# Optimization experiments

Measured on AMD Instinct MI355X. Metric: run time of the kernel, lower is better.

## Reference

```python
import jax, jax.numpy as jnp
import numpy as np

N_NODES = 50000
EMBED = 64
N_EDGES = 1250000
N_USERS = 25000
BATCH, K = 1024, 100


def setup_inputs() -> dict:
    key = jax.random.key(0)
    ks = jax.random.split(key, 8)
    stdv = 1.0 / np.sqrt(EMBED)
    emb = jax.random.uniform(ks[0], (N_NODES, EMBED), jnp.float32, -stdv, stdv)
    # nn.Linear default init: U(-1/sqrt(fan_in), 1/sqrt(fan_in))
    lim = 1.0 / np.sqrt(EMBED)
    W0 = jax.random.uniform(ks[1], (EMBED, EMBED), jnp.float32, -lim, lim)
    b0 = jax.random.uniform(ks[2], (EMBED,), jnp.float32, -lim, lim)
    W1 = jax.random.uniform(ks[3], (EMBED, EMBED), jnp.float32, -lim, lim)
    b1 = jax.random.uniform(ks[4], (EMBED,), jnp.float32, -lim, lim)
    src = jax.random.randint(ks[5], (N_EDGES,), 0, N_NODES, jnp.int32)
    dst = jax.random.randint(ks[6], (N_EDGES,), 0, N_NODES, jnp.int32)
    user_index = jax.random.randint(ks[7], (BATCH, K), 0, N_USERS, jnp.int32)
    item_index = jax.random.randint(jax.random.fold_in(key, 99), (BATCH, K), 0, N_NODES, jnp.int32)
    return {"embeddings": emb, "W0": W0, "b0": b0, "W1": W1, "b1": b1,
            "src": src, "dst": dst, "user_index": user_index, "item_index": item_index}


def _mean_aggregate(h, src, dst):
    # copy_src gather + mailbox mean: mean of src features over incoming edges per dst
    msg_sum = jax.ops.segment_sum(h[src], dst, num_segments=N_NODES)  # [N, D]
    deg = jax.ops.segment_sum(jnp.ones((src.shape[0],), h.dtype), dst, num_segments=N_NODES)
    return msg_sum / jnp.maximum(deg, 1.0)[:, None]


def reference(embeddings, W0, b0, W1, b1, src, dst, user_index, item_index):
    h = embeddings
    for W, b in ((W0, b0), (W1, b1)):
        agg = _mean_aggregate(h, src, dst)          # [N, D] mean mailbox
        h = jnp.tanh(agg @ W.T + b)                  # NodeUpdate: Linear + Tanh
    user = h[user_index]                             # [B, K, D]
    item = h[item_index]                             # [B, K, D]
    score = jnp.sum(user * item, axis=2)             # [B, K]
    return score
```

## Files before the change

kernel.cpp:

```cpp
#include <hip/hip_runtime.h>

#define N_NODES 50000
#define N_EDGES 1250000
#define EMBED 64
#define N_PAIRS (1024 * 100)
#define BSHIFT 7
#define BSIZE 128
#define NBUCK 391
#define CB 153
#define LDS_CAP 4096
#define GEMV_BLKS ((N_NODES + 63) / 64)

__device__ inline float bf2f(unsigned short u) {
    return __uint_as_float(((unsigned)u) << 16);
}
__device__ inline unsigned short f2bf(float x) {
    unsigned u = __float_as_uint(x);
    u += 0x7FFF + ((u >> 16) & 1);
    return (unsigned short)(u >> 16);
}

__global__ __launch_bounds__(1024) void hist_kernel(const int* __restrict__ dst,
                                                    int* __restrict__ counts) {
    __shared__ int hl[NBUCK];
    int t = threadIdx.x, b = blockIdx.x;
    for (int i = t; i < NBUCK; i += 1024) hl[i] = 0;
    __syncthreads();
    #pragma unroll
    for (int rep = 0; rep < 2; ++rep) {
        int i4 = b * 2048 + rep * 1024 + t;
        if (i4 < N_EDGES / 4) {
            int4 d = ((const int4*)dst)[i4];
            atomicAdd(&hl[d.x >> BSHIFT], 1);
            atomicAdd(&hl[d.y >> BSHIFT], 1);
            atomicAdd(&hl[d.z >> BSHIFT], 1);
            atomicAdd(&hl[d.w >> BSHIFT], 1);
        }
    }
    __syncthreads();
    for (int i = t; i < NBUCK; i += 1024) counts[i * CB + b] = hl[i];
}

__global__ __launch_bounds__(512) void prep_kernel(const int* __restrict__ counts,
                                                   int* __restrict__ offs,
                                                   int* __restrict__ base) {
    __shared__ int ws[8];
    int t = threadIdx.x, lane = t & 63, wid = t >> 6;
    const int* rowp = counts + (size_t)t * CB;
    int tot = 0;
    if (t < NBUCK)
        for (int b = 0; b < CB; ++b) tot += rowp[b];
    int incl = tot;
    #pragma unroll
    for (int off = 1; off < 64; off <<= 1) {
        int o = __shfl_up(incl, off);
        if (lane >= off) incl += o;
    }
    if (lane == 63) ws[wid] = incl;
    __syncthreads();
    if (t < 8) {
        int x = ws[t];
        #pragma unroll
        for (int off = 1; off < 8; off <<= 1) {
            int o = __shfl_up(x, off);
            if (t >= off) x += o;
        }
        ws[t] = x;
    }
    __syncthreads();
    int ex = ((wid > 0) ? ws[wid - 1] : 0) + incl - tot;
    if (t < NBUCK) base[t] = ex;
    if (t == 0) base[NBUCK] = N_EDGES;
    if (t < NBUCK) {
        int run = ex;
        int* orow = offs + (size_t)t * CB;
        for (int b = 0; b < CB; ++b) {
            orow[b] = run;
            run += rowp[b];
        }
    }
}

__global__ __launch_bounds__(1024) void scatter_kernel(const int* __restrict__ src,
                                                       const int* __restrict__ dst,
                                                       const int* __restrict__ offs,
                                                       unsigned int* __restrict__ pairs) {
    __shared__ int cur[NBUCK];
    int t = threadIdx.x, b = blockIdx.x;
    for (int i = t; i < NBUCK; i += 1024) cur[i] = offs[i * CB + b];
    __syncthreads();
    #pragma unroll
    for (int rep = 0; rep < 2; ++rep) {
        int i4 = b * 2048 + rep * 1024 + t;
        if (i4 < N_EDGES / 4) {
            int4 s4 = ((const int4*)src)[i4];
            int4 d4 = ((const int4*)dst)[i4];
            int p;
            p = atomicAdd(&cur[d4.x >> BSHIFT], 1);
            pairs[p] = ((unsigned)(d4.x & (BSIZE - 1)) << 16) | (unsigned)s4.x;
            p = atomicAdd(&cur[d4.y >> BSHIFT], 1);
            pairs[p] = ((unsigned)(d4.y & (BSIZE - 1)) << 16) | (unsigned)s4.y;
            p = atomicAdd(&cur[d4.z >> BSHIFT], 1);
            pairs[p] = ((unsigned)(d4.z & (BSIZE - 1)) << 16) | (unsigned)s4.z;
            p = atomicAdd(&cur[d4.w >> BSHIFT], 1);
            pairs[p] = ((unsigned)(d4.w & (BSIZE - 1)) << 16) | (unsigned)s4.w;
        }
    }
}

#define SMEM_BYTES 33808
__global__ __launch_bounds__(256) void sortgemv_kernel(const unsigned int* __restrict__ pairs,
                                                       const int* __restrict__ base,
                                                       int* __restrict__ row,
                                                       int* __restrict__ col,
                                                       const float* __restrict__ emb,
                                                       const float* __restrict__ W,
                                                       unsigned short* __restrict__ g) {
    __shared__ __align__(16) char smem[SMEM_BYTES];
    int t = threadIdx.x;
    if (blockIdx.x < NBUCK) {
        unsigned* ebuf = (unsigned*)smem;
        int* staged    = (int*)(smem + 16384);
        int* hist      = (int*)(smem + 32768);
        int* cur       = (int*)(smem + 33280);
        int* wtot      = (int*)(smem + 33792);
        int k = blockIdx.x;
        int lane = t & 63, wid = t >> 6;
        int nstart = k * BSIZE;
        int nodes = min(BSIZE, N_NODES - nstart);
        int estart = base[k], eend = base[k + 1];
        int cnt = eend - estart;
        if (t < BSIZE) hist[t] = 0;
        __syncthreads();
        if (cnt <= LDS_CAP) {
            for (int i = t; i < cnt; i += 256) {
                unsigned w = pairs[estart + i];
                ebuf[i] = w;
                atomicAdd(&hist[w >> 16], 1);
            }
            __syncthreads();
            if (t < BSIZE) {
                int v = hist[t];
                int incl = v;
                #pragma unroll
                for (int off = 1; off < 64; off <<= 1) {
                    int o = __shfl_up(incl, off);
                    if (lane >= off) incl += o;
                }
                if (t == 63) *wtot = incl;
                __syncthreads();
                int ex = incl - v + ((wid == 1) ? *wtot : 0);
                cur[t] = ex;
                if (t < nodes) row[nstart + t] = estart + ex;
            } else {
                __syncthreads();
            }
            if (k == NBUCK - 1 && t == 0) row[N_NODES] = N_EDGES;
            __syncthreads();
            for (int i = t; i < cnt; i += 256) {
                unsigned w = ebuf[i];
                int pos = atomicAdd(&cur[w >> 16], 1);
                staged[pos] = (int)(w & 0xFFFFu);
            }
            __syncthreads();
            for (int i = t; i < cnt; i += 256) col[estart + i] = staged[i];
        } else {
            for (int i = t; i < cnt; i += 256)
                atomicAdd(&hist[pairs[estart + i] >> 16], 1);
            __syncthreads();
            if (t < BSIZE) {
                int v = hist[t];
                int incl = v;
                #pragma unroll
                for (int off = 1; off < 64; off <<= 1) {
                    int o = __shfl_up(incl, off);
                    if (lane >= off) incl += o;
                }
                if (t == 63) *wtot = incl;
                __syncthreads();
                int ex = incl - v + ((wid == 1) ? *wtot : 0);
                cur[t] = ex;
                if (t < nodes) row[nstart + t] = estart + ex;
            } else {
                __syncthreads();
            }
            if (k == NBUCK - 1 && t == 0) row[N_NODES] = N_EDGES;
            __syncthreads();
            for (int i = t; i < cnt; i += 256) {
                unsigned w = pairs[estart + i];
                int pos = atomicAdd(&cur[w >> 16], 1);
                col[estart + pos] = (int)(w & 0xFFFFu);
            }
        }
    } else {
        float (*hL)[64] = (float (*)[64])smem;
        float (*Wl)[65] = (float (*)[65])(smem + 16384);
        int nstart = (blockIdx.x - NBUCK) * 64;
        int lane = t & 63, wid = t >> 6;
        for (int i = t; i < 4096; i += 256) Wl[i & 63][i >> 6] = W[i];
        int nrem = min(64, N_NODES - nstart);
        for (int i = t; i < nrem * 16; i += 256)
            ((float4*)hL)[i] = ((const float4*)(emb + (size_t)nstart * EMBED))[i];
        __syncthreads();
        for (int n = wid; n < nrem; n += 4) {
            float x = 0.f;
            #pragma unroll
            for (int d = 0; d < 64; ++d)
                x += hL[n][d] * Wl[d][lane];
            g[(size_t)(nstart + n) * EMBED + lane] = f2bf(x);
        }
    }
}

__global__ __launch_bounds__(256) void gemv_bf16_kernel(const unsigned short* __restrict__ h,
                                                        const float* __restrict__ W,
                                                        unsigned short* __restrict__ g) {
    __shared__ float hL[64][64];
    __shared__ float Wl[64][65];
    int t = threadIdx.x;
    int nstart = blockIdx.x * 64;
    int lane = t & 63, wid = t >> 6;
    for (int i = t; i < 4096; i += 256) Wl[i & 63][i >> 6] = W[i];
    int nrem = min(64, N_NODES - nstart);
    for (int i = t; i < nrem * 16; i += 256) {
        ushort4 v = ((const ushort4*)(h + (size_t)nstart * EMBED))[i];
        int r = i >> 4, c = (i & 15) * 4;
        hL[r][c + 0] = bf2f(v.x);
        hL[r][c + 1] = bf2f(v.y);
        hL[r][c + 2] = bf2f(v.z);
        hL[r][c + 3] = bf2f(v.w);
    }
    __syncthreads();
    for (int n = wid; n < nrem; n += 4) {
        float x = 0.f;
        #pragma unroll
        for (int d = 0; d < 64; ++d)
            x += hL[n][d] * Wl[d][lane];
        g[(size_t)(nstart + n) * EMBED + lane] = f2bf(x);
    }
}

__global__ __launch_bounds__(256) void agg_kernel(const unsigned short* __restrict__ g,
                                                  const float* __restrict__ bias,
                                                  const int* __restrict__ row,
                                                  const int* __restrict__ col,
                                                  unsigned short* __restrict__ hout) {
    int t = threadIdx.x;
    int wid = t >> 6, lane = t & 63;
    int node = blockIdx.x * 4 + wid;
    int gg = lane >> 4, d16 = lane & 15;
    int start = row[node], end = row[node + 1];
    float4 bb = ((const float4*)bias)[d16];
    float4 acc = {0.f, 0.f, 0.f, 0.f};
    for (int e = start; e < end; e += 32) {
        #pragma unroll
        for (int k = 0; k < 8; ++k) {
            int ee = e + 4 * k + gg;
            if (ee < end) {
                int s = col[ee];
                ushort4 v = ((const ushort4*)(g + (size_t)s * EMBED))[d16];
                acc.x += bf2f(v.x);
                acc.y += bf2f(v.y);
                acc.z += bf2f(v.z);
                acc.w += bf2f(v.w);
            }
        }
    }
    #pragma unroll
    for (int off = 16; off < 64; off <<= 1) {
        acc.x += __shfl_xor(acc.x, off);
        acc.y += __shfl_xor(acc.y, off);
        acc.z += __shfl_xor(acc.z, off);
        acc.w += __shfl_xor(acc.w, off);
    }
    int dg = end - start;
    float inv = (dg > 0) ? 1.0f / (float)dg : 0.f;
    if (gg == 0) {
        ushort4 o;
        o.x = f2bf(tanhf(acc.x * inv + bb.x));
        o.y = f2bf(tanhf(acc.y * inv + bb.y));
        o.z = f2bf(tanhf(acc.z * inv + bb.z));
        o.w = f2bf(tanhf(acc.w * inv + bb.w));
        ((ushort4*)(hout + (size_t)node * EMBED))[d16] = o;
    }
}

__global__ __launch_bounds__(256) void score_kernel(const unsigned short* __restrict__ h,
                                                    const int* __restrict__ ui,
                                                    const int* __restrict__ ii,
                                                    float* __restrict__ out) {
    int t = threadIdx.x;
    int idx = blockIdx.x * 16 + (t >> 4);
    int d16 = t & 15;
    int u = ui[idx];
    int v = ii[idx];
    ushort4 a4 = ((const ushort4*)(h + (size_t)u * EMBED))[d16];
    ushort4 b4 = ((const ushort4*)(h + (size_t)v * EMBED))[d16];
    float p = bf2f(a4.x) * bf2f(b4.x) + bf2f(a4.y) * bf2f(b4.y) +
              bf2f(a4.z) * bf2f(b4.z) + bf2f(a4.w) * bf2f(b4.w);
    #pragma unroll
    for (int off = 8; off > 0; off >>= 1)
        p += __shfl_xor(p, off);
    if (d16 == 0) out[idx] = p;
}

extern "C" void kernel_launch(void* const* d_in, const int* in_sizes, int n_in,
                              void* d_out, int out_size, void* d_ws, size_t ws_size,
                              hipStream_t stream) {
    const float* emb = (const float*)d_in[0];
    const float* W0  = (const float*)d_in[1];
    const float* b0  = (const float*)d_in[2];
    const float* W1  = (const float*)d_in[3];
    const float* b1  = (const float*)d_in[4];
    const int* src   = (const int*)d_in[5];
    const int* dst   = (const int*)d_in[6];
    const int* ui    = (const int*)d_in[7];
    const int* ii    = (const int*)d_in[8];
    float* out = (float*)d_out;

    char* p = (char*)d_ws;
    auto alloc = [&](size_t bytes) {
        char* r = p;
        p += (bytes + 255) & ~(size_t)255;
        return r;
    };
    int* counts          = (int*)alloc(sizeof(int) * NBUCK * CB);
    int* offs            = (int*)alloc(sizeof(int) * NBUCK * CB);
    int* base            = (int*)alloc(sizeof(int) * (NBUCK + 1));
    int* row             = (int*)alloc(sizeof(int) * (N_NODES + 1));
    unsigned* pairs      = (unsigned*)alloc(sizeof(unsigned) * N_EDGES);
    int* col             = (int*)alloc(sizeof(int) * N_EDGES);
    unsigned short* gbuf = (unsigned short*)alloc(sizeof(unsigned short) * N_NODES * EMBED);
    unsigned short* hbuf = (unsigned short*)alloc(sizeof(unsigned short) * N_NODES * EMBED);

    hist_kernel<<<CB, 1024, 0, stream>>>(dst, counts);
    prep_kernel<<<1, 512, 0, stream>>>(counts, offs, base);
    scatter_kernel<<<CB, 1024, 0, stream>>>(src, dst, offs, pairs);
    sortgemv_kernel<<<NBUCK + GEMV_BLKS, 256, 0, stream>>>(pairs, base, row, col,
                                                           emb, W0, gbuf);
    agg_kernel<<<N_NODES / 4, 256, 0, stream>>>(gbuf, b0, row, col, hbuf);
    gemv_bf16_kernel<<<GEMV_BLKS, 256, 0, stream>>>(hbuf, W1, gbuf);
    agg_kernel<<<N_NODES / 4, 256, 0, stream>>>(gbuf, b1, row, col, hbuf);
    score_kernel<<<N_PAIRS / 16, 256, 0, stream>>>(hbuf, ui, ii, out);
}
```

Measured before the change: 257.7 us.

## Parallelize bucket offset scan across blocks with atomic totals and warp scans

The single-block prep kernel is split up. Bucket totals are now accumulated with global atomics in the histogram kernel, a small single-block kernel scans those totals, and a new kernel with one 64-thread block per bucket computes the per-block offsets using wavefront shuffle scans. This removes the serial per-thread loops over 153 entries in one block, which read the counts with strided, uncoalesced access. In exchange it adds a memset and an extra kernel launch, plus global atomics in the histogram.

```diff
diff --git a/kernel.cpp b/kernel.cpp
--- a/kernel.cpp
+++ b/kernel.cpp
@@ -21,7 +21,8 @@
 }
 
 __global__ __launch_bounds__(1024) void hist_kernel(const int* __restrict__ dst,
-                                                    int* __restrict__ counts) {
+                                                    int* __restrict__ counts,
+                                                    int* __restrict__ btot) {
     __shared__ int hl[NBUCK];
     int t = threadIdx.x, b = blockIdx.x;
     for (int i = t; i < NBUCK; i += 1024) hl[i] = 0;
@@ -38,19 +39,19 @@
         }
     }
     __syncthreads();
-    for (int i = t; i < NBUCK; i += 1024) counts[i * CB + b] = hl[i];
-}
-
-__global__ __launch_bounds__(512) void prep_kernel(const int* __restrict__ counts,
-                                                   int* __restrict__ offs,
-                                                   int* __restrict__ base) {
+    for (int i = t; i < NBUCK; i += 1024) {
+        int v = hl[i];
+        counts[i * CB + b] = v;
+        if (v) atomicAdd(&btot[i], v);
+    }
+}
+
+__global__ __launch_bounds__(512) void bscan_kernel(const int* __restrict__ btot,
+                                                    int* __restrict__ base) {
     __shared__ int ws[8];
     int t = threadIdx.x, lane = t & 63, wid = t >> 6;
-    const int* rowp = counts + (size_t)t * CB;
-    int tot = 0;
-    if (t < NBUCK)
-        for (int b = 0; b < CB; ++b) tot += rowp[b];
-    int incl = tot;
+    int v = (t < NBUCK) ? btot[t] : 0;
+    int incl = v;
     #pragma unroll
     for (int off = 1; off < 64; off <<= 1) {
         int o = __shfl_up(incl, off);
@@ -68,16 +69,30 @@
         ws[t] = x;
     }
     __syncthreads();
-    int ex = ((wid > 0) ? ws[wid - 1] : 0) + incl - tot;
+    int ex = ((wid > 0) ? ws[wid - 1] : 0) + incl - v;
     if (t < NBUCK) base[t] = ex;
     if (t == 0) base[NBUCK] = N_EDGES;
-    if (t < NBUCK) {
-        int run = ex;
-        int* orow = offs + (size_t)t * CB;
-        for (int b = 0; b < CB; ++b) {
-            orow[b] = run;
-            run += rowp[b];
-        }
+}
+
+__global__ __launch_bounds__(64) void offs_kernel(const int* __restrict__ counts,
+                                                  const int* __restrict__ base,
+                                                  int* __restrict__ offs) {
+    int k = blockIdx.x, lane = threadIdx.x;
+    const int* rowp = counts + (size_t)k * CB;
+    int* orow = offs + (size_t)k * CB;
+    int carry = base[k];
+    #pragma unroll
+    for (int tile = 0; tile < 3; ++tile) {
+        int b = tile * 64 + lane;
+        int v = (b < CB) ? rowp[b] : 0;
+        int incl = v;
+        #pragma unroll
+        for (int off = 1; off < 64; off <<= 1) {
+            int o = __shfl_up(incl, off);
+            if (lane >= off) incl += o;
+        }
+        if (b < CB) orow[b] = carry + incl - v;
+        carry += __shfl(incl, 63);
     }
 }
 
@@ -326,6 +341,7 @@
     };
     int* counts          = (int*)alloc(sizeof(int) * NBUCK * CB);
     int* offs            = (int*)alloc(sizeof(int) * NBUCK * CB);
+    int* btot            = (int*)alloc(sizeof(int) * NBUCK);
     int* base            = (int*)alloc(sizeof(int) * (NBUCK + 1));
     int* row             = (int*)alloc(sizeof(int) * (N_NODES + 1));
     unsigned* pairs      = (unsigned*)alloc(sizeof(unsigned) * N_EDGES);
@@ -333,8 +349,10 @@
     unsigned short* gbuf = (unsigned short*)alloc(sizeof(unsigned short) * N_NODES * EMBED);
     unsigned short* hbuf = (unsigned short*)alloc(sizeof(unsigned short) * N_NODES * EMBED);
 
-    hist_kernel<<<CB, 1024, 0, stream>>>(dst, counts);
-    prep_kernel<<<1, 512, 0, stream>>>(counts, offs, base);
+    hipMemsetAsync(btot, 0, sizeof(int) * NBUCK, stream);
+    hist_kernel<<<CB, 1024, 0, stream>>>(dst, counts, btot);
+    bscan_kernel<<<1, 512, 0, stream>>>(btot, base);
+    offs_kernel<<<NBUCK, 64, 0, stream>>>(counts, base, offs);
     scatter_kernel<<<CB, 1024, 0, stream>>>(src, dst, offs, pairs);
     sortgemv_kernel<<<NBUCK + GEMV_BLKS, 256, 0, stream>>>(pairs, base, row, col,
                                                            emb, W0, gbuf);
```

Result: faster. 245.9 us (-4.6%).
